# Kernel optimization log

Measured on AMD Instinct MI355X. Metric: run time of the kernel, lower is better.

Reference implementation:

```python
import jax, jax.numpy as jnp
import numpy as np
from functools import partial

B, INPUT_DIM, CHUNK, D, NLAYERS, FF, NCLS = 16, 20480, 10, 256, 4, 1024, 10
L = INPUT_DIM // CHUNK  # 2048
FILT_EMB, FILT_HID = 16, 64
EPS = 1e-5


def sinusoidal_pe(length, dim):
    pos = jnp.arange(length, dtype=jnp.float32)[:, None]
    div = jnp.exp(jnp.arange(0, dim, 2, dtype=jnp.float32) * (-np.log(10000.0) / dim))
    ang = pos * div  # (length, dim//2)
    pe = jnp.zeros((length, dim), dtype=jnp.float32)
    pe = pe.at[:, 0::2].set(jnp.sin(ang)).at[:, 1::2].set(jnp.cos(ang))
    return pe


def layernorm(x, g, b):
    mu = jnp.mean(x, axis=-1, keepdims=True)
    var = jnp.mean(jnp.square(x - mu), axis=-1, keepdims=True)
    return (x - mu) * jax.lax.rsqrt(var + EPS) * g + b


def setup_inputs() -> dict:
    key = jax.random.key(0)
    ks = iter(jax.random.split(key, 32))
    s = 0.02
    r = lambda shape: jax.random.normal(next(ks), shape, dtype=jnp.float32) * s
    inp = {
        'x': jax.random.normal(next(ks), (B, INPUT_DIM), dtype=jnp.float32),
        'inp_w': r((CHUNK, D)), 'inp_b': jnp.zeros((D,)),
        'in_proj_w': r((NLAYERS, D, 3 * D)), 'in_proj_b': jnp.zeros((NLAYERS, 3 * D)),
        'short_w': r((NLAYERS, D, 3)), 'short_b': jnp.zeros((NLAYERS, D)),
        'filt_w1': r((NLAYERS, FILT_EMB, FILT_HID)), 'filt_b1': jnp.zeros((NLAYERS, FILT_HID)),
        'filt_w2': r((NLAYERS, FILT_HID, D)), 'filt_b2': jnp.zeros((NLAYERS, D)),
        'out_w': r((NLAYERS, D, D)), 'out_b': jnp.zeros((NLAYERS, D)),
        'ln1_g': jnp.ones((NLAYERS, D)), 'ln1_b': jnp.zeros((NLAYERS, D)),
        'ln2_g': jnp.ones((NLAYERS, D)), 'ln2_b': jnp.zeros((NLAYERS, D)),
        'ffn_w1': r((NLAYERS, D, FF)), 'ffn_b1': jnp.zeros((NLAYERS, FF)),
        'ffn_w2': r((NLAYERS, FF, D)), 'ffn_b2': jnp.zeros((NLAYERS, D)),
        'norm_g': jnp.ones((D,)), 'norm_b': jnp.zeros((D,)),
        'cls_w': r((D, NCLS)), 'cls_b': jnp.zeros((NCLS,)),
    }
    return inp


def _hyena_op(u, in_w, in_b, sw, sb, fw1, fb1, fw2, fb2, ow, ob, pe16):
    # u: (B, L, D)
    proj = u @ in_w + in_b                       # (B, L, 3D)
    x0, x1, x2 = jnp.split(proj, 3, axis=-1)
    # depthwise short conv, kernel 3, same padding
    x0t = jnp.transpose(x0, (0, 2, 1))           # (B, D, L)
    x0c = jax.lax.conv_general_dilated(
        x0t, sw[:, None, :], window_strides=(1,), padding=[(1, 1)],
        feature_group_count=D, dimension_numbers=('NCH', 'OIH', 'NCH'))
    x0c = jnp.transpose(x0c + sb[None, :, None], (0, 2, 1))  # (B, L, D)
    # implicit long filter from positional MLP
    h = jax.nn.gelu(pe16 @ fw1 + fb1, approximate=False) @ fw2 + fb2  # (L, D)
    # FFT causal-style long conv (n = 2L)
    xf = jnp.fft.rfft(x0c, n=2 * L, axis=1)
    hf = jnp.fft.rfft(h, n=2 * L, axis=0)
    y = jnp.fft.irfft(xf * hf[None], n=2 * L, axis=1)[:, :L, :]
    y = y * x1 * x2                              # elementwise gating
    return y @ ow + ob


def reference(x, inp_w, inp_b, in_proj_w, in_proj_b, short_w, short_b,
              filt_w1, filt_b1, filt_w2, filt_b2, out_w, out_b,
              ln1_g, ln1_b, ln2_g, ln2_b, ffn_w1, ffn_b1, ffn_w2, ffn_b2,
              norm_g, norm_b, cls_w, cls_b):
    xs = x.reshape(B, L, CHUNK) @ inp_w + inp_b  # (B, L, D)
    xs = xs + sinusoidal_pe(L, D)[None]
    pe16 = sinusoidal_pe(L, FILT_EMB)
    for i in range(NLAYERS):
        h = _hyena_op(layernorm(xs, ln1_g[i], ln1_b[i]),
                      in_proj_w[i], in_proj_b[i], short_w[i], short_b[i],
                      filt_w1[i], filt_b1[i], filt_w2[i], filt_b2[i],
                      out_w[i], out_b[i], pe16)
        xs = xs + h
        z = layernorm(xs, ln2_g[i], ln2_b[i])
        z = jax.nn.gelu(z @ ffn_w1[i] + ffn_b1[i], approximate=False) @ ffn_w2[i] + ffn_b2[i]
        xs = xs + z
    pooled = layernorm(jnp.mean(xs, axis=1), norm_g, norm_b)
    return pooled @ cls_w + cls_b
```

## Files before the change

kernel.cpp:

```cpp
#include <hip/hip_runtime.h>
#include <math.h>

#define BB 16
#define LL 2048
#define CHUNK 10
#define DD 256
#define NLAYERS 4
#define FFD 1024
#define NCLS 10
#define HSTRC 2056

typedef short bf16x8 __attribute__((ext_vector_type(8)));
typedef short s16x4 __attribute__((ext_vector_type(4)));
typedef float f32x4 __attribute__((ext_vector_type(4)));

__device__ __forceinline__ unsigned short f2bf(float f) {
    unsigned int u = __builtin_bit_cast(unsigned int, f);
    u = (u + 0x7FFF + ((u >> 16) & 1)) >> 16;
    return (unsigned short)u;
}
__device__ __forceinline__ float bf2f(unsigned short s) {
    unsigned int u = ((unsigned int)s) << 16;
    return __builtin_bit_cast(float, u);
}
__device__ __forceinline__ float bfLO(unsigned v) { return __builtin_bit_cast(float, v << 16); }
__device__ __forceinline__ float bfHI(unsigned v) { return __builtin_bit_cast(float, v & 0xFFFF0000u); }

#define PADC(a) ((a) + ((a) >> 4))

__device__ __forceinline__ float2 cmulf(float2 a, float2 b) {
    return make_float2(fmaf(-a.y, b.y, a.x * b.x), fmaf(a.y, b.x, a.x * b.y));
}

#define GLL16(gsrc, ldst) \
    __builtin_amdgcn_global_load_lds((const __attribute__((address_space(1))) void*)(gsrc), \
                                     (__attribute__((address_space(3))) void*)(ldst), 16, 0, 0)

__global__ __launch_bounds__(256)
void embed_k(const float* __restrict__ x, const float* __restrict__ iw,
             const float* __restrict__ ib, unsigned short* __restrict__ xsb)
{
    const int tid = threadIdx.x;
    const size_t row0 = (size_t)blockIdx.x * 8;
    const int i2 = (tid >> 1) * 2;
    const float div = expf(-0.03597789207803197f * (float)i2);
    float wcol[CHUNK];
#pragma unroll
    for (int c = 0; c < CHUNK; ++c) wcol[c] = iw[c * DD + tid];
    const float bv = ib[tid];
    for (int rr = 0; rr < 8; ++rr) {
        size_t row = row0 + rr;
        int l = (int)(row & (LL - 1));
        const float* xr = x + row * CHUNK;
        float acc = bv;
#pragma unroll
        for (int c = 0; c < CHUNK; ++c) acc += xr[c] * wcol[c];
        float sv, cv;
        sincosf((float)l * div, &sv, &cv);
        acc += (tid & 1) ? cv : sv;
        xsb[row * DD + tid] = f2bf(acc);
    }
}

__global__ __launch_bounds__(256)
void filt_all_k(const float* __restrict__ fw1, const float* __restrict__ fb1,
                const float* __restrict__ fw2, const float* __restrict__ fb2,
                float* __restrict__ hTall)
{
    __shared__ float pe[16];
    __shared__ float hid[64];
    const int tid = threadIdx.x;
    const int layer = blockIdx.x >> 11;
    const int l = blockIdx.x & 2047;
    const float* w1 = fw1 + layer * 1024;
    const float* b1 = fb1 + layer * 64;
    const float* w2 = fw2 + layer * 16384;
    const float* b2 = fb2 + layer * 256;
    if (tid < 16) {
        int i2 = (tid >> 1) * 2;
        float div = expf(-0.5756462732485114f * (float)i2);
        float sv, cv;
        sincosf((float)l * div, &sv, &cv);
        pe[tid] = (tid & 1) ? cv : sv;
    }
    __syncthreads();
    if (tid < 64) {
        float a = b1[tid];
#pragma unroll
        for (int e = 0; e < 16; ++e) a += pe[e] * w1[e * 64 + tid];
        hid[tid] = 0.5f * a * (1.0f + erff(a * 0.70710678118f));
    }
    __syncthreads();
    float a = b2[tid];
#pragma unroll
    for (int h = 0; h < 64; ++h) a += hid[h] * w2[h * DD + tid];
    hTall[(size_t)layer * 524288 + (size_t)tid * LL + l] = a;
}

__device__ __forceinline__ void dft4c(float2 a, float2 b, float2 c, float2 d,
                                      float2& F0, float2& F1, float2& F2, float2& F3)
{
    float t0r = a.x + c.x, t0i = a.y + c.y;
    float t1r = a.x - c.x, t1i = a.y - c.y;
    float t2r = b.x + d.x, t2i = b.y + d.y;
    float t3r = b.x - d.x, t3i = b.y - d.y;
    F0 = make_float2(t0r + t2r, t0i + t2i);
    F2 = make_float2(t0r - t2r, t0i - t2i);
    F1 = make_float2(t1r + t3i, t1i - t3r);
    F3 = make_float2(t1r - t3i, t1i + t3r);
}

template <int SH>
__device__ __forceinline__ void stage8ip(float2* __restrict__ A, int tid)
{
    constexpr int ST = 1 << SH;
    const int p = tid >> SH;
    const int q = tid & (ST - 1);
    float2 x0 = A[PADC(tid)];
    float2 x1 = A[PADC(tid + 256)];
    float2 x2 = A[PADC(tid + 512)];
    float2 x3 = A[PADC(tid + 768)];
    float2 x4 = A[PADC(tid + 1024)];
    float2 x5 = A[PADC(tid + 1280)];
    float2 x6 = A[PADC(tid + 1536)];
    float2 x7 = A[PADC(tid + 1792)];
    float2 E0, E1, E2, E3, O0, O1, O2, O3;
    dft4c(x0, x2, x4, x6, E0, E1, E2, E3);
    dft4c(x1, x3, x5, x7, O0, O1, O2, O3);
    const float C8 = 0.70710678118654752f;
    float2 y0 = make_float2(E0.x + O0.x, E0.y + O0.y);
    float2 y4 = make_float2(E0.x - O0.x, E0.y - O0.y);
    float a1 = C8 * (O1.x + O1.y), b1 = C8 * (O1.y - O1.x);
    float2 y1 = make_float2(E1.x + a1, E1.y + b1);
    float2 y5 = make_float2(E1.x - a1, E1.y - b1);
    float2 y2 = make_float2(E2.x + O2.y, E2.y - O2.x);
    float2 y6 = make_float2(E2.x - O2.y, E2.y + O2.x);
    float a3 = -C8 * (O3.x - O3.y), b3 = -C8 * (O3.x + O3.y);
    float2 y3 = make_float2(E3.x + a3, E3.y + b3);
    float2 y7 = make_float2(E3.x - a3, E3.y - b3);
    const int k0 = p << SH;
    float s1, c1;
    __sincosf(-3.0679615757712823e-3f * (float)k0, &s1, &c1);
    float2 w1 = make_float2(c1, s1);
    float2 w2 = cmulf(w1, w1);
    float2 w3 = cmulf(w2, w1);
    float2 w4 = cmulf(w2, w2);
    float2 w5 = cmulf(w3, w2);
    float2 w6 = cmulf(w3, w3);
    float2 w7 = cmulf(w4, w3);
    float2 o1 = cmulf(w1, y1);
    float2 o2 = cmulf(w2, y2);
    float2 o3 = cmulf(w3, y3);
    float2 o4 = cmulf(w4, y4);
    float2 o5 = cmulf(w5, y5);
    float2 o6 = cmulf(w6, y6);
    float2 o7 = cmulf(w7, y7);
    __syncthreads();
    const int ob = q + ((ST * p) << 3);
    A[PADC(ob)] = y0;
    A[PADC(ob + ST)] = o1;
    A[PADC(ob + 2 * ST)] = o2;
    A[PADC(ob + 3 * ST)] = o3;
    A[PADC(ob + 4 * ST)] = o4;
    A[PADC(ob + 5 * ST)] = o5;
    A[PADC(ob + 6 * ST)] = o6;
    A[PADC(ob + 7 * ST)] = o7;
    __syncthreads();
}

__device__ __forceinline__ void stage4fip(float2* __restrict__ A, int tid)
{
    float2 v[2][4];
#pragma unroll
    for (int jj = 0; jj < 2; ++jj) {
        int u = tid + (jj << 8);
        v[jj][0] = A[PADC(u)];
        v[jj][1] = A[PADC(u + 512)];
        v[jj][2] = A[PADC(u + 1024)];
        v[jj][3] = A[PADC(u + 1536)];
    }
    __syncthreads();
#pragma unroll
    for (int jj = 0; jj < 2; ++jj) {
        int u = tid + (jj << 8);
        float2 F0, F1, F2, F3;
        dft4c(v[jj][0], v[jj][1], v[jj][2], v[jj][3], F0, F1, F2, F3);
        A[PADC(u)] = F0;
        A[PADC(u + 512)] = F1;
        A[PADC(u + 1024)] = F2;
        A[PADC(u + 1536)] = F3;
    }
    __syncthreads();
}

__device__ __forceinline__ void fft2048ip(float2* __restrict__ A, int tid)
{
    stage8ip<0>(A, tid);
    stage8ip<3>(A, tid);
    stage8ip<6>(A, tid);
    stage4fip(A, tid);
}

__global__ __launch_bounds__(256)
void ffth_all_k(const float* __restrict__ hTall, float2* __restrict__ Hfall)
{
    __shared__ float2 A2[2176];
    const int tid = threadIdx.x;
    const int layer = blockIdx.x >> 8;
    const int d = blockIdx.x & 255;
    const float2* rowf = reinterpret_cast<const float2*>(hTall + (size_t)layer * 524288 + (size_t)d * LL);
#pragma unroll
    for (int j = 0; j < 4; ++j) {
        int u = tid + (j << 8);
        A2[PADC(u)] = rowf[u];
        A2[PADC(u + 1024)] = make_float2(0.0f, 0.0f);
    }
    __syncthreads();
    fft2048ip(A2, tid);
    float2* hf = Hfall + ((size_t)layer * 256 + d) * HSTRC;
#pragma unroll
    for (int j = 0; j < 4; ++j) {
        int k = 1 + tid + (j << 8);
        int m = 2048 - k;
        float2 zk = A2[PADC(k)], zm = A2[PADC(m)];
        float Er = 0.5f * (zk.x + zm.x), Ei = 0.5f * (zk.y - zm.y);
        float Or = 0.5f * (zk.y + zm.y), Oi = -0.5f * (zk.x - zm.x);
        float ts, tc;
        __sincosf(-1.5339807878856412e-3f * (float)k, &ts, &tc);
        float TOr = tc * Or - ts * Oi, TOi = tc * Oi + ts * Or;
        hf[k] = make_float2(Er + TOr, Ei + TOi);
        hf[m] = make_float2(Er - TOr, -(Ei - TOi));
    }
    if (tid == 0) {
        float2 z0 = A2[PADC(0)];
        hf[0] = make_float2(z0.x + z0.y, z0.x - z0.y);
    }
}

__global__ __launch_bounds__(256, 4)
void fftconv_k(const unsigned short* __restrict__ x0T, unsigned short* __restrict__ yT,
               const float2* __restrict__ Hf, const float* __restrict__ sw,
               const float* __restrict__ sb)
{
    __shared__ float2 A2[2176];
    const int tid = threadIdx.x;
    const int w = blockIdx.x;
    const int c = w & 7, s = w >> 3;
    const int d = c * 32 + (s & 31);
    const int b = s >> 5;
    const int blk = b * 256 + d;
    const float w0 = sw[d * 3], w1 = sw[d * 3 + 1], w2 = sw[d * 3 + 2];
    const float bv = sb[d];

    float* rawF = reinterpret_cast<float*>(A2);
    {
        const uint4* rowv = reinterpret_cast<const uint4*>(x0T + (size_t)blk * LL);
        uint4 ld = rowv[tid];
        int p = tid << 3;
        int lB = p & ~63;
        int p6 = p & 63;
        int fg = p6 >> 4;
        int m0 = (p6 >> 2) & 3;
        float4* d0 = reinterpret_cast<float4*>(rawF + lB + m0 * 16 + fg * 4);
        float4* d1 = reinterpret_cast<float4*>(rawF + lB + (m0 + 1) * 16 + fg * 4);
        *d0 = make_float4(bfLO(ld.x), bfHI(ld.x), bfLO(ld.y), bfHI(ld.y));
        *d1 = make_float4(bfLO(ld.z), bfHI(ld.z), bfLO(ld.w), bfHI(ld.w));
    }
    __syncthreads();
    float2 zv[4];
#pragma unroll
    for (int j = 0; j < 4; ++j) {
        int u = tid + (j << 8);
        float xm1 = (u == 0) ? 0.0f : rawF[2 * u - 1];
        float xc0 = rawF[2 * u];
        float xp1 = rawF[2 * u + 1];
        float xp2 = (u == 1023) ? 0.0f : rawF[2 * u + 2];
        zv[j].x = bv + w0 * xm1 + w1 * xc0 + w2 * xp1;
        zv[j].y = bv + w0 * xc0 + w1 * xp1 + w2 * xp2;
    }
    __syncthreads();
#pragma unroll
    for (int j = 0; j < 4; ++j) {
        int u = tid + (j << 8);
        A2[PADC(u)] = zv[j];
        A2[PADC(u + 1024)] = make_float2(0.0f, 0.0f);
    }
    __syncthreads();
    fft2048ip(A2, tid);
    const float2* hf = Hf + (size_t)d * HSTRC;
#pragma unroll
    for (int j = 0; j < 4; ++j) {
        int k = 1 + tid + (j << 8);
        int m = 2048 - k;
        float2 zk = A2[PADC(k)], zm = A2[PADC(m)];
        float Er = 0.5f * (zk.x + zm.x), Ei = 0.5f * (zk.y - zm.y);
        float Or = 0.5f * (zk.y + zm.y), Oi = -0.5f * (zk.x - zm.x);
        float ts, tc;
        __sincosf(-1.5339807878856412e-3f * (float)k, &ts, &tc);
        float TOr = tc * Or - ts * Oi, TOi = tc * Oi + ts * Or;
        float Xpr = Er + TOr, Xpi = Ei + TOi;
        float Xmr = Er - TOr, Xmi = Ei - TOi;
        float2 hk = hf[k], hm = hf[m];
        float Ykr = Xpr * hk.x - Xpi * hk.y, Yki = Xpr * hk.y + Xpi * hk.x;
        float Cr = Xmr * hm.x + Xmi * hm.y, Ci = Xmi * hm.x - Xmr * hm.y;
        float Pr = 0.5f * (Ykr + Cr), Pi = 0.5f * (Yki + Ci);
        float Gr = 0.5f * (Ykr - Cr), Gi = 0.5f * (Yki - Ci);
        float Qr = tc * Gr + ts * Gi, Qi = tc * Gi - ts * Gr;
        A2[PADC(k)] = make_float2(Pr - Qi, -(Pi + Qr));
        A2[PADC(m)] = make_float2(Pr + Qi, Pi - Qr);
    }
    if (tid == 0) {
        float2 z0 = A2[PADC(0)];
        float2 h0 = hf[0];
        float X0 = z0.x + z0.y, X2 = z0.x - z0.y;
        float Y0 = X0 * h0.x, Y2 = X2 * h0.y;
        float P = 0.5f * (Y0 + Y2), Q = 0.5f * (Y0 - Y2);
        A2[PADC(0)] = make_float2(P, -Q);
    }
    __syncthreads();
    fft2048ip(A2, tid);
    const float sc = 1.0f / 2048.0f;
    unsigned* yrow = reinterpret_cast<unsigned*>(yT + (size_t)blk * LL);
#pragma unroll
    for (int j = 0; j < 4; ++j) {
        int u = tid + (j << 8);
        float2 v = A2[PADC(u)];
        float e = v.x * sc, o = -v.y * sc;
        yrow[u] = (unsigned)f2bf(e) | ((unsigned)f2bf(o) << 16);
    }
}

__global__ __launch_bounds__(256)
void gate_k(const unsigned short* __restrict__ yTb, const unsigned short* __restrict__ px,
            unsigned short* __restrict__ yg)
{
    __shared__ float t[64][65];
    const int tid = threadIdx.x;
    const int blk = blockIdx.x;
    const int b = blk >> 7;
    const int dt = (blk >> 5) & 3;
    const int lt = blk & 31;
    const int d0 = dt << 6, l0 = lt << 6;
    const int r0 = tid >> 6, c = tid & 63;
    for (int rr = 0; rr < 16; ++rr) {
        int dl = rr * 4 + r0;
        t[dl][c] = bf2f(yTb[(((size_t)(b << 8) + d0 + dl) << 11) + l0 + c]);
    }
    __syncthreads();
    const int lid = tid & 63, lr = tid >> 6;
    for (int k = 0; k < 16; ++k) {
        int ll = k * 4 + lr;
        int l = l0 + ll;
        size_t pb = ((size_t)(b * LL + l)) * 512;
        float v = t[lid][ll];
        float x1 = bf2f(px[pb + d0 + lid]);
        float x2 = bf2f(px[pb + 256 + d0 + lid]);
        yg[((size_t)(b * LL + l)) * DD + d0 + lid] = f2bf(v * x1 * x2);
    }
}

__global__ __launch_bounds__(256)
void lncast_k(const unsigned short* __restrict__ xsb, const float* __restrict__ g,
              const float* __restrict__ b, unsigned short* __restrict__ o)
{
    const int tid = threadIdx.x, lane = tid & 63, wave = tid >> 6;
    const size_t row = (size_t)blockIdx.x * 4 + wave;
    s16x4 vv = reinterpret_cast<const s16x4*>(xsb + row * DD)[lane];
    float v0 = bf2f((unsigned short)vv[0]), v1 = bf2f((unsigned short)vv[1]);
    float v2 = bf2f((unsigned short)vv[2]), v3 = bf2f((unsigned short)vv[3]);
    float s = v0 + v1 + v2 + v3;
#pragma unroll
    for (int off = 32; off > 0; off >>= 1) s += __shfl_xor(s, off, 64);
    float mean = s * (1.0f / 256.0f);
    float e0 = v0 - mean, e1 = v1 - mean, e2 = v2 - mean, e3 = v3 - mean;
    float q = e0 * e0 + e1 * e1 + e2 * e2 + e3 * e3;
#pragma unroll
    for (int off = 32; off > 0; off >>= 1) q += __shfl_xor(q, off, 64);
    float rstd = rsqrtf(q * (1.0f / 256.0f) + 1e-5f);
    float4 gg = reinterpret_cast<const float4*>(g)[lane];
    float4 bb = reinterpret_cast<const float4*>(b)[lane];
    s16x4 r;
    r[0] = (short)f2bf(e0 * rstd * gg.x + bb.x);
    r[1] = (short)f2bf(e1 * rstd * gg.y + bb.y);
    r[2] = (short)f2bf(e2 * rstd * gg.z + bb.z);
    r[3] = (short)f2bf(e3 * rstd * gg.w + bb.w);
    *reinterpret_cast<s16x4*>(o + row * DD + lane * 4) = r;
}

__global__ __launch_bounds__(256)
void wcast_all_k(const float* __restrict__ in_proj_w, const float* __restrict__ out_w,
                 const float* __restrict__ ffn_w1, const float* __restrict__ ffn_w2,
                 unsigned short* __restrict__ WTb)
{
    const int bid = blockIdx.x;
    const int layer = bid / 768;
    const int r = bid % 768;
    const float* W; unsigned short* WT; int K, N, nt, kt;
    unsigned short* wt = WTb + (size_t)layer * 786432;
    if (r < 192)      { int i = r;       nt = i % 24; kt = i / 24; K = 256;  N = 768;
                        W = in_proj_w + (size_t)layer * 196608; WT = wt; }
    else if (r < 256) { int i = r - 192; nt = i % 8;  kt = i / 8;  K = 256;  N = 256;
                        W = out_w + (size_t)layer * 65536;      WT = wt + 196608; }
    else if (r < 512) { int i = r - 256; nt = i % 32; kt = i / 32; K = 256;  N = 1024;
                        W = ffn_w1 + (size_t)layer * 262144;    WT = wt + 262144; }
    else              { int i = r - 512; nt = i % 8;  kt = i / 8;  K = 1024; N = 256;
                        W = ffn_w2 + (size_t)layer * 262144;    WT = wt + 524288; }
    __shared__ float t[32][33];
    const int tx = threadIdx.x & 31, ty = threadIdx.x >> 5;
    const int n0 = nt * 32, k0 = kt * 32;
#pragma unroll
    for (int j = 0; j < 4; ++j)
        t[ty + 8 * j][tx] = W[(size_t)(k0 + ty + 8 * j) * N + n0 + tx];
    __syncthreads();
#pragma unroll
    for (int j = 0; j < 4; ++j)
        WT[(size_t)(n0 + ty + 8 * j) * K + k0 + tx] = f2bf(t[tx][ty + 8 * j]);
}

template <int K, int N, int MODE>
__global__ __launch_bounds__(256)
void gemm_k(const unsigned short* __restrict__ A, const unsigned short* __restrict__ WT,
            const float* __restrict__ bias, void* __restrict__ outp, void* __restrict__ outp2)
{
    constexpr int C = N / 128;
    __shared__ unsigned short ldsA[8192];
    __shared__ unsigned short ldsB[8192];
    const int tid = threadIdx.x;
    const int lane = tid & 63, wid = tid >> 6;
    const int nwg = gridDim.x;
    const int w = blockIdx.x;
    const int logical = (w & 7) * (nwg >> 3) + (w >> 3);
    const int row0 = (logical / C) * 128;
    const int col0 = (logical % C) * 128;
    const int wm = (wid >> 1) * 64, wn = (wid & 1) * 64;
    const int fr = lane & 15, fg = lane >> 4;

    f32x4 acc[4][4];
#pragma unroll
    for (int n = 0; n < 4; ++n) {
        float bv = bias[col0 + wn + n * 16 + fr];
#pragma unroll
        for (int m = 0; m < 4; ++m) {
            acc[m][n][0] = bv; acc[m][n][1] = bv; acc[m][n][2] = bv; acc[m][n][3] = bv;
        }
    }

    const int srow = wid * 8 + (lane >> 3);
    const int sc = lane & 7;

    for (int kt = 0; kt < K / 64; ++kt) {
        const int k0 = kt * 64;
#pragma unroll
        for (int it = 0; it < 4; ++it) {
            int row = it * 32 + srow;
            int cs = sc ^ (row & 7);
            const char* ga = (const char*)(A + (size_t)(row0 + row) * K + k0) + cs * 16;
            const char* gb = (const char*)(WT + (size_t)(col0 + row) * K + k0) + cs * 16;
            GLL16(ga, (char*)ldsA + it * 4096 + wid * 1024);
            GLL16(gb, (char*)ldsB + it * 4096 + wid * 1024);
        }
        __syncthreads();
#pragma unroll
        for (int ks = 0; ks < 2; ++ks) {
            bf16x8 af[4], bf[4];
#pragma unroll
            for (int m = 0; m < 4; ++m) {
                int ar = wm + m * 16 + fr;
                int slot = (ks * 4 + fg) ^ (ar & 7);
                af[m] = *reinterpret_cast<const bf16x8*>(ldsA + ar * 64 + slot * 8);
            }
#pragma unroll
            for (int n = 0; n < 4; ++n) {
                int br = wn + n * 16 + fr;
                int slot = (ks * 4 + fg) ^ (br & 7);
                bf[n] = *reinterpret_cast<const bf16x8*>(ldsB + br * 64 + slot * 8);
            }
#pragma unroll
            for (int m = 0; m < 4; ++m)
#pragma unroll
                for (int n = 0; n < 4; ++n)
                    acc[m][n] = __builtin_amdgcn_mfma_f32_16x16x32_bf16(af[m], bf[n], acc[m][n], 0, 0, 0);
        }
        __syncthreads();
    }

    if constexpr (MODE == 3) {
        if (col0 < 256) {
            const int b = row0 >> 11;
            const int lb0 = (row0 & (LL - 1)) + wm;
#pragma unroll
            for (int n = 0; n < 4; ++n) {
                int dcol = col0 + wn + n * 16 + fr;
                unsigned short* dst = (unsigned short*)outp +
                    (((size_t)(b << 8) + dcol) << 11) + lb0 + fg * 16;
                unsigned pk[8];
#pragma unroll
                for (int q = 0; q < 8; ++q) {
                    int m = q >> 1, r0 = (q & 1) * 2;
                    pk[q] = (unsigned)f2bf(acc[m][n][r0]) | ((unsigned)f2bf(acc[m][n][r0 + 1]) << 16);
                }
                *reinterpret_cast<uint4*>(dst)     = make_uint4(pk[0], pk[1], pk[2], pk[3]);
                *reinterpret_cast<uint4*>(dst + 8) = make_uint4(pk[4], pk[5], pk[6], pk[7]);
            }
        } else {
            unsigned short* px = (unsigned short*)outp2;
#pragma unroll
            for (int m = 0; m < 4; ++m) {
                int gr = row0 + wm + m * 16 + fg * 4;
#pragma unroll
                for (int n = 0; n < 4; ++n) {
                    int gc = col0 - 256 + wn + n * 16 + fr;
#pragma unroll
                    for (int r = 0; r < 4; ++r)
                        px[(size_t)(gr + r) * 512 + gc] = f2bf(acc[m][n][r]);
                }
            }
        }
        return;
    }

#pragma unroll
    for (int m = 0; m < 4; ++m) {
        int gr = row0 + wm + m * 16 + fg * 4;
#pragma unroll
        for (int n = 0; n < 4; ++n) {
            int gc = col0 + wn + n * 16 + fr;
#pragma unroll
            for (int r = 0; r < 4; ++r) {
                float v = acc[m][n][r];
                if constexpr (MODE == 1) v = 0.5f * v * (1.0f + erff(v * 0.70710678118f));
                if constexpr (MODE <= 1) {
                    ((unsigned short*)outp)[(size_t)(gr + r) * N + gc] = f2bf(v);
                } else {
                    unsigned short* o = (unsigned short*)outp + (size_t)(gr + r) * N + gc;
                    *o = f2bf(bf2f(*o) + v);
                }
            }
        }
    }
}

template <int K>
__global__ __launch_bounds__(256)
void gemm_ln_k(const unsigned short* __restrict__ A, const unsigned short* __restrict__ WT,
               const float* __restrict__ bias, const float* __restrict__ lng,
               const float* __restrict__ lnb, unsigned short* __restrict__ xsb,
               unsigned short* __restrict__ xln)
{
    __shared__ unsigned short ldsA[64 * 64];
    __shared__ unsigned short ldsB[256 * 64];
    const int tid = threadIdx.x;
    const int lane = tid & 63, wid = tid >> 6;
    const int nwg = gridDim.x;
    const int w = blockIdx.x;
    const int logical = (w & 7) * (nwg >> 3) + (w >> 3);
    const size_t row0 = (size_t)logical * 64;
    const int fr = lane & 15, fg = lane >> 4;

    f32x4 acc[16];
#pragma unroll
    for (int n = 0; n < 16; ++n) {
        float bv = bias[n * 16 + fr];
        acc[n][0] = bv; acc[n][1] = bv; acc[n][2] = bv; acc[n][3] = bv;
    }

    for (int kt = 0; kt < K / 64; ++kt) {
        const int k0 = kt * 64;
#pragma unroll
        for (int p = 0; p < 2; ++p) {
            int cch = p * 256 + tid;
            int row = cch >> 3;
            int cs = (cch & 7) ^ (row & 7);
            const char* ga = (const char*)(A + (row0 + row) * K + k0) + cs * 16;
            GLL16(ga, (char*)ldsA + p * 4096 + wid * 1024);
        }
#pragma unroll
        for (int p = 0; p < 8; ++p) {
            int cch = p * 256 + tid;
            int row = cch >> 3;
            int cs = (cch & 7) ^ (row & 7);
            const char* gb = (const char*)(WT + (size_t)row * K + k0) + cs * 16;
            GLL16(gb, (char*)ldsB + p * 4096 + wid * 1024);
        }
        __syncthreads();
#pragma unroll
        for (int ks = 0; ks < 2; ++ks) {
            int ar = wid * 16 + fr;
            int slotA = (ks * 4 + fg) ^ (ar & 7);
            bf16x8 af = *reinterpret_cast<const bf16x8*>(ldsA + ar * 64 + slotA * 8);
#pragma unroll
            for (int n = 0; n < 16; ++n) {
                int br = n * 16 + fr;
                int slotB = (ks * 4 + fg) ^ (br & 7);
                bf16x8 bf = *reinterpret_cast<const bf16x8*>(ldsB + br * 64 + slotB * 8);
                acc[n] = __builtin_amdgcn_mfma_f32_16x16x32_bf16(af, bf, acc[n], 0, 0, 0);
            }
        }
        __syncthreads();
    }

    const size_t rbase = row0 + wid * 16 + fg * 4;
#pragma unroll
    for (int r = 0; r < 4; ++r) {
        const unsigned short* xr = xsb + (rbase + r) * DD;
#pragma unroll
        for (int n = 0; n < 16; ++n)
            acc[n][r] += bf2f(xr[fr + 16 * n]);
    }
    float sm[4], sq[4];
#pragma unroll
    for (int r = 0; r < 4; ++r) {
        float s = 0.0f, q = 0.0f;
#pragma unroll
        for (int n = 0; n < 16; ++n) {
            float v = acc[n][r];
            s += v; q += v * v;
        }
#pragma unroll
        for (int off = 1; off < 16; off <<= 1) {
            s += __shfl_xor(s, off, 64);
            q += __shfl_xor(q, off, 64);
        }
        sm[r] = s * (1.0f / 256.0f);
        float var = q * (1.0f / 256.0f) - sm[r] * sm[r];
        sq[r] = rsqrtf(var + 1e-5f);
    }
    float gv[16], bvv[16];
#pragma unroll
    for (int n = 0; n < 16; ++n) {
        gv[n] = lng[fr + 16 * n];
        bvv[n] = lnb[fr + 16 * n];
    }
#pragma unroll
    for (int r = 0; r < 4; ++r) {
        unsigned short* xw = xsb + (rbase + r) * DD;
        unsigned short* lw = xln + (rbase + r) * DD;
#pragma unroll
        for (int n = 0; n < 16; ++n) {
            int gc = fr + 16 * n;
            float v = acc[n][r];
            xw[gc] = f2bf(v);
            lw[gc] = f2bf((v - sm[r]) * sq[r] * gv[n] + bvv[n]);
        }
    }
}

__global__ __launch_bounds__(256)
void pool_k(const unsigned short* __restrict__ xsb, float* __restrict__ part)
{
    const int tid = threadIdx.x;
    const int b = blockIdx.x >> 4, g = blockIdx.x & 15;
    size_t base = ((size_t)b * LL + g * 128) * DD + tid;
    float s = 0.0f;
    for (int l = 0; l < 128; ++l) s += bf2f(xsb[base + (size_t)l * DD]);
    part[(size_t)blockIdx.x * DD + tid] = s;
}

__global__ __launch_bounds__(256)
void final_k(const float* __restrict__ part, const float* __restrict__ ng,
             const float* __restrict__ nb, const float* __restrict__ cw,
             const float* __restrict__ cb, float* __restrict__ out)
{
    __shared__ float pl[256];
    __shared__ float red[4], red2[4];
    const int tid = threadIdx.x, b = blockIdx.x;
    float m = 0.0f;
    for (int g = 0; g < 16; ++g) m += part[((size_t)b * 16 + g) * DD + tid];
    m *= (1.0f / (float)LL);
    const int lane = tid & 63, wave = tid >> 6;
    float s = m;
#pragma unroll
    for (int off = 32; off > 0; off >>= 1) s += __shfl_xor(s, off, 64);
    if (lane == 0) red[wave] = s;
    __syncthreads();
    float mean = (red[0] + red[1] + red[2] + red[3]) * (1.0f / 256.0f);
    float dm = m - mean;
    float qv = dm * dm;
#pragma unroll
    for (int off = 32; off > 0; off >>= 1) qv += __shfl_xor(qv, off, 64);
    if (lane == 0) red2[wave] = qv;
    __syncthreads();
    float var = (red2[0] + red2[1] + red2[2] + red2[3]) * (1.0f / 256.0f);
    pl[tid] = dm * rsqrtf(var + 1e-5f) * ng[tid] + nb[tid];
    __syncthreads();
    if (tid < NCLS) {
        float a = cb[tid];
        for (int dd = 0; dd < 256; ++dd) a += pl[dd] * cw[dd * NCLS + tid];
        out[b * NCLS + tid] = a;
    }
}

extern "C" void kernel_launch(void* const* d_in, const int* in_sizes, int n_in,
                              void* d_out, int out_size, void* d_ws, size_t ws_size,
                              hipStream_t stream)
{
    (void)in_sizes; (void)n_in; (void)out_size; (void)ws_size;
    const float* x        = (const float*)d_in[0];
    const float* inp_w    = (const float*)d_in[1];
    const float* inp_b    = (const float*)d_in[2];
    const float* in_proj_w= (const float*)d_in[3];
    const float* in_proj_b= (const float*)d_in[4];
    const float* short_w  = (const float*)d_in[5];
    const float* short_b  = (const float*)d_in[6];
    const float* filt_w1  = (const float*)d_in[7];
    const float* filt_b1  = (const float*)d_in[8];
    const float* filt_w2  = (const float*)d_in[9];
    const float* filt_b2  = (const float*)d_in[10];
    const float* out_w    = (const float*)d_in[11];
    const float* out_b    = (const float*)d_in[12];
    const float* ln1_g    = (const float*)d_in[13];
    const float* ln1_b    = (const float*)d_in[14];
    const float* ln2_g    = (const float*)d_in[15];
    const float* ln2_b    = (const float*)d_in[16];
    const float* ffn_w1   = (const float*)d_in[17];
    const float* ffn_b1   = (const float*)d_in[18];
    const float* ffn_w2   = (const float*)d_in[19];
    const float* ffn_b2   = (const float*)d_in[20];
    const float* norm_g   = (const float*)d_in[21];
    const float* norm_b   = (const float*)d_in[22];
    const float* cls_w    = (const float*)d_in[23];
    const float* cls_b    = (const float*)d_in[24];

    float* ws = (float*)d_ws;
    unsigned short* xsb  = (unsigned short*)ws;
    unsigned short* xln  = (unsigned short*)(ws + 4194304);
    unsigned short* x0T  = (unsigned short*)(ws + 8388608);
    unsigned short* yT   = (unsigned short*)(ws + 12582912);
    unsigned short* projx= (unsigned short*)(ws + 16777216);
    unsigned short* ygp  = x0T;
    unsigned short* hid  = x0T;
    float* hTall         = ws + 25165824;
    float2* Hfall        = (float2*)(ws + 27262976);
    float* part          = ws + 31473664;
    unsigned short* WTb  = (unsigned short*)(ws + 31539200);

    wcast_all_k<<<3072, 256, 0, stream>>>(in_proj_w, out_w, ffn_w1, ffn_w2, WTb);
    embed_k<<<4096, 256, 0, stream>>>(x, inp_w, inp_b, xsb);
    lncast_k<<<8192, 256, 0, stream>>>(xsb, ln1_g, ln1_b, xln);
    filt_all_k<<<NLAYERS * 2048, 256, 0, stream>>>(filt_w1, filt_b1, filt_w2, filt_b2, hTall);
    ffth_all_k<<<NLAYERS * 256, 256, 0, stream>>>(hTall, Hfall);

    for (int i = 0; i < NLAYERS; ++i) {
        unsigned short* wt = WTb + (size_t)i * 786432;
        float2* Hf = Hfall + (size_t)i * 256 * HSTRC;
        gemm_k<256, 768, 3><<<1536, 256, 0, stream>>>(
            xln, wt, in_proj_b + i * 768, x0T, projx);
        fftconv_k<<<4096, 256, 0, stream>>>(x0T, yT, Hf, short_w + i * 768, short_b + i * 256);
        gate_k<<<2048, 256, 0, stream>>>(yT, projx, ygp);
        gemm_ln_k<256><<<512, 256, 0, stream>>>(
            ygp, wt + 196608, out_b + i * 256, ln2_g + i * 256, ln2_b + i * 256, xsb, xln);
        gemm_k<256, 1024, 1><<<2048, 256, 0, stream>>>(
            xln, wt + 262144, ffn_b1 + i * 1024, hid, nullptr);
        if (i < NLAYERS - 1) {
            gemm_ln_k<1024><<<512, 256, 0, stream>>>(
                hid, wt + 524288, ffn_b2 + i * 256,
                ln1_g + (i + 1) * 256, ln1_b + (i + 1) * 256, xsb, xln);
        } else {
            gemm_k<1024, 256, 2><<<512, 256, 0, stream>>>(
                hid, wt + 524288, ffn_b2 + i * 256, xsb, nullptr);
        }
    }

    pool_k<<<BB * 16, 256, 0, stream>>>(xsb, part);
    final_k<<<BB, 256, 0, stream>>>(part, norm_g, norm_b, cls_w, cls_b, (float*)d_out);
}
```

Measured before the change: 682.0 us.

## Pack two real channels per complex 4096-point FFT in fftconv

Before, each block ran a 2048-point complex FFT over one channel, using the even/odd real-FFT packing trick, which needs twiddle-based split and merge steps. Now each block packs two adjacent channels as the real and imaginary parts of one 4096-point complex FFT. The spectrum is separated by conjugate symmetry, each half is multiplied by its own filter spectrum, and both are recombined before a single inverse FFT, so the twiddle post-processing disappears and the grid is halved. In exchange, shared memory per block doubles, which can lower occupancy, each thread now does a radix-8 stage covering two butterflies, and the bf16 output stores are now 16-bit scalar writes instead of packed 32-bit ones.

```diff
diff --git a/kernel.cpp b/kernel.cpp
--- a/kernel.cpp
+++ b/kernel.cpp
@@ -110,34 +110,34 @@
     F3 = make_float2(t1r - t3i, t1i + t3r);
 }
 
+__device__ __forceinline__ void bfly8(const float2* x, float2* y)
+{
+    float2 E0, E1, E2, E3, O0, O1, O2, O3;
+    dft4c(x[0], x[2], x[4], x[6], E0, E1, E2, E3);
+    dft4c(x[1], x[3], x[5], x[7], O0, O1, O2, O3);
+    const float C8 = 0.70710678118654752f;
+    y[0] = make_float2(E0.x + O0.x, E0.y + O0.y);
+    y[4] = make_float2(E0.x - O0.x, E0.y - O0.y);
+    float a1 = C8 * (O1.x + O1.y), b1 = C8 * (O1.y - O1.x);
+    y[1] = make_float2(E1.x + a1, E1.y + b1);
+    y[5] = make_float2(E1.x - a1, E1.y - b1);
+    y[2] = make_float2(E2.x + O2.y, E2.y - O2.x);
+    y[6] = make_float2(E2.x - O2.y, E2.y + O2.x);
+    float a3 = -C8 * (O3.x - O3.y), b3 = -C8 * (O3.x + O3.y);
+    y[3] = make_float2(E3.x + a3, E3.y + b3);
+    y[7] = make_float2(E3.x - a3, E3.y - b3);
+}
+
 template <int SH>
 __device__ __forceinline__ void stage8ip(float2* __restrict__ A, int tid)
 {
     constexpr int ST = 1 << SH;
     const int p = tid >> SH;
     const int q = tid & (ST - 1);
-    float2 x0 = A[PADC(tid)];
-    float2 x1 = A[PADC(tid + 256)];
-    float2 x2 = A[PADC(tid + 512)];
-    float2 x3 = A[PADC(tid + 768)];
-    float2 x4 = A[PADC(tid + 1024)];
-    float2 x5 = A[PADC(tid + 1280)];
-    float2 x6 = A[PADC(tid + 1536)];
-    float2 x7 = A[PADC(tid + 1792)];
-    float2 E0, E1, E2, E3, O0, O1, O2, O3;
-    dft4c(x0, x2, x4, x6, E0, E1, E2, E3);
-    dft4c(x1, x3, x5, x7, O0, O1, O2, O3);
-    const float C8 = 0.70710678118654752f;
-    float2 y0 = make_float2(E0.x + O0.x, E0.y + O0.y);
-    float2 y4 = make_float2(E0.x - O0.x, E0.y - O0.y);
-    float a1 = C8 * (O1.x + O1.y), b1 = C8 * (O1.y - O1.x);
-    float2 y1 = make_float2(E1.x + a1, E1.y + b1);
-    float2 y5 = make_float2(E1.x - a1, E1.y - b1);
-    float2 y2 = make_float2(E2.x + O2.y, E2.y - O2.x);
-    float2 y6 = make_float2(E2.x - O2.y, E2.y + O2.x);
-    float a3 = -C8 * (O3.x - O3.y), b3 = -C8 * (O3.x + O3.y);
-    float2 y3 = make_float2(E3.x + a3, E3.y + b3);
-    float2 y7 = make_float2(E3.x - a3, E3.y - b3);
+    float2 x[8], y[8];
+#pragma unroll
+    for (int i = 0; i < 8; ++i) x[i] = A[PADC(tid + (i << 8))];
+    bfly8(x, y);
     const int k0 = p << SH;
     float s1, c1;
     __sincosf(-3.0679615757712823e-3f * (float)k0, &s1, &c1);
@@ -148,16 +148,16 @@
     float2 w5 = cmulf(w3, w2);
     float2 w6 = cmulf(w3, w3);
     float2 w7 = cmulf(w4, w3);
-    float2 o1 = cmulf(w1, y1);
-    float2 o2 = cmulf(w2, y2);
-    float2 o3 = cmulf(w3, y3);
-    float2 o4 = cmulf(w4, y4);
-    float2 o5 = cmulf(w5, y5);
-    float2 o6 = cmulf(w6, y6);
-    float2 o7 = cmulf(w7, y7);
+    float2 o1 = cmulf(w1, y[1]);
+    float2 o2 = cmulf(w2, y[2]);
+    float2 o3 = cmulf(w3, y[3]);
+    float2 o4 = cmulf(w4, y[4]);
+    float2 o5 = cmulf(w5, y[5]);
+    float2 o6 = cmulf(w6, y[6]);
+    float2 o7 = cmulf(w7, y[7]);
     __syncthreads();
     const int ob = q + ((ST * p) << 3);
-    A[PADC(ob)] = y0;
+    A[PADC(ob)] = y[0];
     A[PADC(ob + ST)] = o1;
     A[PADC(ob + 2 * ST)] = o2;
     A[PADC(ob + 3 * ST)] = o3;
@@ -199,6 +199,56 @@
     stage8ip<3>(A, tid);
     stage8ip<6>(A, tid);
     stage4fip(A, tid);
+}
+
+template <int SH>
+__device__ __forceinline__ void stage8ip4(float2* __restrict__ A, int tid)
+{
+    constexpr int ST = 1 << SH;
+    float2 x[2][8];
+#pragma unroll
+    for (int j = 0; j < 2; ++j) {
+        int u = tid + (j << 8);
+#pragma unroll
+        for (int i = 0; i < 8; ++i) x[j][i] = A[PADC(u + (i << 9))];
+    }
+    __syncthreads();
+#pragma unroll
+    for (int j = 0; j < 2; ++j) {
+        int u = tid + (j << 8);
+        const int p = u >> SH;
+        const int q = u & (ST - 1);
+        float2 y[8];
+        bfly8(x[j], y);
+        const int k0 = p << SH;
+        float s1, c1;
+        __sincosf(-1.5339807878856412e-3f * (float)k0, &s1, &c1);
+        float2 w1 = make_float2(c1, s1);
+        float2 w2 = cmulf(w1, w1);
+        float2 w3 = cmulf(w2, w1);
+        float2 w4 = cmulf(w2, w2);
+        float2 w5 = cmulf(w3, w2);
+        float2 w6 = cmulf(w3, w3);
+        float2 w7 = cmulf(w4, w3);
+        const int ob = q + ((ST * p) << 3);
+        A[PADC(ob)] = y[0];
+        A[PADC(ob + ST)] = cmulf(w1, y[1]);
+        A[PADC(ob + 2 * ST)] = cmulf(w2, y[2]);
+        A[PADC(ob + 3 * ST)] = cmulf(w3, y[3]);
+        A[PADC(ob + 4 * ST)] = cmulf(w4, y[4]);
+        A[PADC(ob + 5 * ST)] = cmulf(w5, y[5]);
+        A[PADC(ob + 6 * ST)] = cmulf(w6, y[6]);
+        A[PADC(ob + 7 * ST)] = cmulf(w7, y[7]);
+    }
+    __syncthreads();
+}
+
+__device__ __forceinline__ void fft4096ip(float2* __restrict__ A, int tid)
+{
+    stage8ip4<0>(A, tid);
+    stage8ip4<3>(A, tid);
+    stage8ip4<6>(A, tid);
+    stage8ip4<9>(A, tid);
 }
 
 __global__ __launch_bounds__(256)
@@ -242,91 +292,100 @@
                const float2* __restrict__ Hf, const float* __restrict__ sw,
                const float* __restrict__ sb)
 {
-    __shared__ float2 A2[2176];
+    __shared__ float2 A2[4352];
     const int tid = threadIdx.x;
     const int w = blockIdx.x;
     const int c = w & 7, s = w >> 3;
-    const int d = c * 32 + (s & 31);
-    const int b = s >> 5;
-    const int blk = b * 256 + d;
-    const float w0 = sw[d * 3], w1 = sw[d * 3 + 1], w2 = sw[d * 3 + 2];
-    const float bv = sb[d];
-
-    float* rawF = reinterpret_cast<float*>(A2);
+    const int d0 = c * 32 + (s & 15) * 2;
+    const int b = s >> 4;
+    const int blk0 = b * 256 + d0;
+    const float wa0 = sw[d0 * 3],     wa1 = sw[d0 * 3 + 1], wa2 = sw[d0 * 3 + 2];
+    const float wb0 = sw[d0 * 3 + 3], wb1 = sw[d0 * 3 + 4], wb2 = sw[d0 * 3 + 5];
+    const float ba = sb[d0], bb = sb[d0 + 1];
+
+    float* rawA = reinterpret_cast<float*>(A2);
+    float* rawB = rawA + 2048;
     {
-        const uint4* rowv = reinterpret_cast<const uint4*>(x0T + (size_t)blk * LL);
-        uint4 ld = rowv[tid];
+        const uint4* rva = reinterpret_cast<const uint4*>(x0T + (size_t)blk0 * LL);
+        const uint4* rvb = reinterpret_cast<const uint4*>(x0T + (size_t)(blk0 + 1) * LL);
+        uint4 la = rva[tid];
+        uint4 lb = rvb[tid];
         int p = tid << 3;
         int lB = p & ~63;
         int p6 = p & 63;
         int fg = p6 >> 4;
         int m0 = (p6 >> 2) & 3;
-        float4* d0 = reinterpret_cast<float4*>(rawF + lB + m0 * 16 + fg * 4);
-        float4* d1 = reinterpret_cast<float4*>(rawF + lB + (m0 + 1) * 16 + fg * 4);
-        *d0 = make_float4(bfLO(ld.x), bfHI(ld.x), bfLO(ld.y), bfHI(ld.y));
-        *d1 = make_float4(bfLO(ld.z), bfHI(ld.z), bfLO(ld.w), bfHI(ld.w));
-    }
-    __syncthreads();
-    float2 zv[4];
-#pragma unroll
-    for (int j = 0; j < 4; ++j) {
-        int u = tid + (j << 8);
-        float xm1 = (u == 0) ? 0.0f : rawF[2 * u - 1];
-        float xc0 = rawF[2 * u];
-        float xp1 = rawF[2 * u + 1];
-        float xp2 = (u == 1023) ? 0.0f : rawF[2 * u + 2];
-        zv[j].x = bv + w0 * xm1 + w1 * xc0 + w2 * xp1;
-        zv[j].y = bv + w0 * xc0 + w1 * xp1 + w2 * xp2;
-    }
-    __syncthreads();
-#pragma unroll
-    for (int j = 0; j < 4; ++j) {
-        int u = tid + (j << 8);
-        A2[PADC(u)] = zv[j];
-        A2[PADC(u + 1024)] = make_float2(0.0f, 0.0f);
-    }
-    __syncthreads();
-    fft2048ip(A2, tid);
-    const float2* hf = Hf + (size_t)d * HSTRC;
-#pragma unroll
-    for (int j = 0; j < 4; ++j) {
+        float4* da0 = reinterpret_cast<float4*>(rawA + lB + m0 * 16 + fg * 4);
+        float4* da1 = reinterpret_cast<float4*>(rawA + lB + (m0 + 1) * 16 + fg * 4);
+        *da0 = make_float4(bfLO(la.x), bfHI(la.x), bfLO(la.y), bfHI(la.y));
+        *da1 = make_float4(bfLO(la.z), bfHI(la.z), bfLO(la.w), bfHI(la.w));
+        float4* db0 = reinterpret_cast<float4*>(rawB + lB + m0 * 16 + fg * 4);
+        float4* db1 = reinterpret_cast<float4*>(rawB + lB + (m0 + 1) * 16 + fg * 4);
+        *db0 = make_float4(bfLO(lb.x), bfHI(lb.x), bfLO(lb.y), bfHI(lb.y));
+        *db1 = make_float4(bfLO(lb.z), bfHI(lb.z), bfLO(lb.w), bfHI(lb.w));
+    }
+    __syncthreads();
+    float2 zv[8];
+#pragma unroll
+    for (int j = 0; j < 8; ++j) {
+        int n = tid + (j << 8);
+        float am1 = (n == 0) ? 0.0f : rawA[n - 1];
+        float ac  = rawA[n];
+        float ap1 = (n == 2047) ? 0.0f : rawA[n + 1];
+        float bm1 = (n == 0) ? 0.0f : rawB[n - 1];
+        float bc  = rawB[n];
+        float bp1 = (n == 2047) ? 0.0f : rawB[n + 1];
+        zv[j].x = ba + wa0 * am1 + wa1 * ac + wa2 * ap1;
+        zv[j].y = bb + wb0 * bm1 + wb1 * bc + wb2 * bp1;
+    }
+    __syncthreads();
+#pragma unroll
+    for (int j = 0; j < 8; ++j) {
+        int n = tid + (j << 8);
+        A2[PADC(n)] = zv[j];
+        A2[PADC(n + 2048)] = make_float2(0.0f, 0.0f);
+    }
+    __syncthreads();
+    fft4096ip(A2, tid);
+    const float2* hfa = Hf + (size_t)d0 * HSTRC;
+    const float2* hfb = hfa + HSTRC;
+#pragma unroll
+    for (int j = 0; j < 8; ++j) {
         int k = 1 + tid + (j << 8);
-        int m = 2048 - k;
-        float2 zk = A2[PADC(k)], zm = A2[PADC(m)];
-        float Er = 0.5f * (zk.x + zm.x), Ei = 0.5f * (zk.y - zm.y);
-        float Or = 0.5f * (zk.y + zm.y), Oi = -0.5f * (zk.x - zm.x);
-        float ts, tc;
-        __sincosf(-1.5339807878856412e-3f * (float)k, &ts, &tc);
-        float TOr = tc * Or - ts * Oi, TOi = tc * Oi + ts * Or;
-        float Xpr = Er + TOr, Xpi = Ei + TOi;
-        float Xmr = Er - TOr, Xmi = Ei - TOi;
-        float2 hk = hf[k], hm = hf[m];
-        float Ykr = Xpr * hk.x - Xpi * hk.y, Yki = Xpr * hk.y + Xpi * hk.x;
-        float Cr = Xmr * hm.x + Xmi * hm.y, Ci = Xmi * hm.x - Xmr * hm.y;
-        float Pr = 0.5f * (Ykr + Cr), Pi = 0.5f * (Yki + Ci);
-        float Gr = 0.5f * (Ykr - Cr), Gi = 0.5f * (Yki - Ci);
-        float Qr = tc * Gr + ts * Gi, Qi = tc * Gi - ts * Gr;
-        A2[PADC(k)] = make_float2(Pr - Qi, -(Pi + Qr));
-        A2[PADC(m)] = make_float2(Pr + Qi, Pi - Qr);
+        if (k < 2048) {
+            int m = 4096 - k;
+            float2 Zk = A2[PADC(k)], Zm = A2[PADC(m)];
+            float Ar = 0.5f * (Zk.x + Zm.x), Ai = 0.5f * (Zk.y - Zm.y);
+            float Br = 0.5f * (Zk.y + Zm.y), Bi = -0.5f * (Zk.x - Zm.x);
+            float2 ha = hfa[k], hb = hfb[k];
+            float Yar = Ar * ha.x - Ai * ha.y, Yai = Ar * ha.y + Ai * ha.x;
+            float Ybr = Br * hb.x - Bi * hb.y, Ybi = Br * hb.y + Bi * hb.x;
+            A2[PADC(k)] = make_float2(Yar - Ybi, -(Yai + Ybr));
+            A2[PADC(m)] = make_float2(Yar + Ybi, Yai - Ybr);
+        } else {
+            float2 Z = A2[PADC(2048)];
+            float Ya = Z.x * hfa[0].y;
+            float Yb = Z.y * hfb[0].y;
+            A2[PADC(2048)] = make_float2(Ya, -Yb);
+        }
     }
     if (tid == 0) {
-        float2 z0 = A2[PADC(0)];
-        float2 h0 = hf[0];
-        float X0 = z0.x + z0.y, X2 = z0.x - z0.y;
-        float Y0 = X0 * h0.x, Y2 = X2 * h0.y;
-        float P = 0.5f * (Y0 + Y2), Q = 0.5f * (Y0 - Y2);
-        A2[PADC(0)] = make_float2(P, -Q);
-    }
-    __syncthreads();
-    fft2048ip(A2, tid);
-    const float sc = 1.0f / 2048.0f;
-    unsigned* yrow = reinterpret_cast<unsigned*>(yT + (size_t)blk * LL);
-#pragma unroll
-    for (int j = 0; j < 4; ++j) {
-        int u = tid + (j << 8);
-        float2 v = A2[PADC(u)];
-        float e = v.x * sc, o = -v.y * sc;
-        yrow[u] = (unsigned)f2bf(e) | ((unsigned)f2bf(o) << 16);
+        float2 Z = A2[PADC(0)];
+        float Ya = Z.x * hfa[0].x;
+        float Yb = Z.y * hfb[0].x;
+        A2[PADC(0)] = make_float2(Ya, -Yb);
+    }
+    __syncthreads();
+    fft4096ip(A2, tid);
+    const float sc = 1.0f / 4096.0f;
+    unsigned short* ya = yT + (size_t)blk0 * LL;
+    unsigned short* yb = ya + LL;
+#pragma unroll
+    for (int j = 0; j < 8; ++j) {
+        int n = tid + (j << 8);
+        float2 v = A2[PADC(n)];
+        ya[n] = f2bf(v.x * sc);
+        yb[n] = f2bf(-v.y * sc);
     }
 }
 
@@ -745,7 +804,7 @@
         float2* Hf = Hfall + (size_t)i * 256 * HSTRC;
         gemm_k<256, 768, 3><<<1536, 256, 0, stream>>>(
             xln, wt, in_proj_b + i * 768, x0T, projx);
-        fftconv_k<<<4096, 256, 0, stream>>>(x0T, yT, Hf, short_w + i * 768, short_b + i * 256);
+        fftconv_k<<<2048, 256, 0, stream>>>(x0T, yT, Hf, short_w + i * 768, short_b + i * 256);
         gate_k<<<2048, 256, 0, stream>>>(yT, projx, ygp);
         gemm_ln_k<256><<<512, 256, 0, stream>>>(
             ygp, wt + 196608, out_b + i * 256, ln2_g + i * 256, ln2_b + i * 256, xsb, xln);
```

Measured after the change: 1.599 ms. +134.4%, slower.

## Fuse x1*x2 gating product into in-projection GEMM epilogue

Applied to the files above, without the earlier changes.

The in-projection GEMM now pairs x1 and x2 column tiles in the same workgroup by remapping B-operand rows and bias indices, so each 128-column tile holds 64 x1 and 64 x2 columns. The two halves are multiplied in the epilogue through an LDS exchange, and a single 256-wide gate tensor is written. The later gating kernel then reads one bf16 value per element instead of two. This halves the gate write and read traffic, at the cost of an extra barrier and LDS round trip in the epilogue, plus rounding the product to bf16 once.

```diff
diff --git a/kernel.cpp b/kernel.cpp
--- a/kernel.cpp
+++ b/kernel.cpp
@@ -351,11 +351,10 @@
     for (int k = 0; k < 16; ++k) {
         int ll = k * 4 + lr;
         int l = l0 + ll;
-        size_t pb = ((size_t)(b * LL + l)) * 512;
+        size_t pb = ((size_t)(b * LL + l)) * 256;
         float v = t[lid][ll];
-        float x1 = bf2f(px[pb + d0 + lid]);
-        float x2 = bf2f(px[pb + 256 + d0 + lid]);
-        yg[((size_t)(b * LL + l)) * DD + d0 + lid] = f2bf(v * x1 * x2);
+        float g = bf2f(px[pb + d0 + lid]);
+        yg[((size_t)(b * LL + l)) * DD + d0 + lid] = f2bf(v * g);
     }
 }
 
@@ -438,7 +437,18 @@
     f32x4 acc[4][4];
 #pragma unroll
     for (int n = 0; n < 4; ++n) {
-        float bv = bias[col0 + wn + n * 16 + fr];
+        int bcol;
+        if constexpr (MODE == 3) {
+            if (col0 >= 256) {
+                int j64 = (col0 - 256) >> 1;
+                bcol = (wn == 0 ? 256 : 512) + j64 + n * 16 + fr;
+            } else {
+                bcol = col0 + wn + n * 16 + fr;
+            }
+        } else {
+            bcol = col0 + wn + n * 16 + fr;
+        }
+        float bv = bias[bcol];
 #pragma unroll
         for (int m = 0; m < 4; ++m) {
             acc[m][n][0] = bv; acc[m][n][1] = bv; acc[m][n][2] = bv; acc[m][n][3] = bv;
@@ -455,9 +465,20 @@
             int row = it * 32 + srow;
             int cs = sc ^ (row & 7);
             const char* ga = (const char*)(A + (size_t)(row0 + row) * K + k0) + cs * 16;
-            const char* gb = (const char*)(WT + (size_t)(col0 + row) * K + k0) + cs * 16;
+            const unsigned short* bsrc;
+            if constexpr (MODE == 3) {
+                if (col0 >= 256) {
+                    int j64 = (col0 - 256) >> 1;
+                    int brow = 256 + ((it >> 1) << 8) + j64 + ((it & 1) << 5) + srow;
+                    bsrc = WT + (size_t)brow * K + k0;
+                } else {
+                    bsrc = WT + (size_t)(col0 + row) * K + k0;
+                }
+            } else {
+                bsrc = WT + (size_t)(col0 + row) * K + k0;
+            }
             GLL16(ga, (char*)ldsA + it * 4096 + wid * 1024);
-            GLL16(gb, (char*)ldsB + it * 4096 + wid * 1024);
+            GLL16((const char*)bsrc + cs * 16, (char*)ldsB + it * 4096 + wid * 1024);
         }
         __syncthreads();
 #pragma unroll
@@ -503,17 +524,34 @@
                 *reinterpret_cast<uint4*>(dst + 8) = make_uint4(pk[4], pk[5], pk[6], pk[7]);
             }
         } else {
-            unsigned short* px = (unsigned short*)outp2;
-#pragma unroll
-            for (int m = 0; m < 4; ++m) {
-                int gr = row0 + wm + m * 16 + fg * 4;
-#pragma unroll
-                for (int n = 0; n < 4; ++n) {
-                    int gc = col0 - 256 + wn + n * 16 + fr;
-#pragma unroll
-                    for (int r = 0; r < 4; ++r)
-                        px[(size_t)(gr + r) * 512 + gc] = f2bf(acc[m][n][r]);
-                }
+            unsigned short* exch = ldsB;
+            if (wn == 64) {
+#pragma unroll
+                for (int m = 0; m < 4; ++m)
+#pragma unroll
+                    for (int n = 0; n < 4; ++n)
+#pragma unroll
+                        for (int r = 0; r < 4; ++r) {
+                            int row = wm + m * 16 + fg * 4 + r;
+                            int ccol = n * 16 + fr;
+                            exch[row * 64 + ccol] = f2bf(acc[m][n][r]);
+                        }
+            }
+            __syncthreads();
+            if (wn == 0) {
+                unsigned short* px = (unsigned short*)outp2;
+                const int j64 = (col0 - 256) >> 1;
+#pragma unroll
+                for (int m = 0; m < 4; ++m)
+#pragma unroll
+                    for (int n = 0; n < 4; ++n)
+#pragma unroll
+                        for (int r = 0; r < 4; ++r) {
+                            int row = wm + m * 16 + fg * 4 + r;
+                            int ccol = n * 16 + fr;
+                            float xp = acc[m][n][r] * bf2f(exch[row * 64 + ccol]);
+                            px[(size_t)(row0 + row) * 256 + j64 + ccol] = f2bf(xp);
+                        }
             }
         }
         return;
```

Result: no change. 691.9 us (+1.5%).
